# Kernel optimization log

Hardware: AMD Instinct MI355X
Metric: run time of the kernel (lower is better)

Reference implementation:

```python
import jax, jax.numpy as jnp
import numpy as np

N_NODES = 50000
N_EDGES = 800000
N_GRAPHS = 64
NEG_SLOPE = 0.2  # PyG GATConv leaky_relu default


def gat_conv(x, src, dst, W, a_src, a_dst, b, concat):
    # PyG GATConv (eval mode): h = W x -> [N,H,C]; e_ij = leakyrelu(a_src.h_j + a_dst.h_i)
    # softmax over incoming edges of each dst node; out_i = sum_j alpha_ij h_j
    N = x.shape[0]
    H, C = a_src.shape
    h = (x @ W).reshape(N, H, C)
    score_s = (h * a_src).sum(-1)  # [N,H]
    score_d = (h * a_dst).sum(-1)  # [N,H]
    e = jax.nn.leaky_relu(score_s[src] + score_d[dst], NEG_SLOPE)  # [E,H]
    m = jax.ops.segment_max(e, dst, num_segments=N)  # [N,H]
    ex = jnp.exp(e - m[dst])
    denom = jax.ops.segment_sum(ex, dst, num_segments=N)  # [N,H], >0 due to self loops
    alpha = ex / denom[dst]
    out = jax.ops.segment_sum(h[src] * alpha[..., None], dst, num_segments=N)  # [N,H,C]
    out = out.reshape(N, H * C) if concat else out.mean(axis=1)
    return out + b


def setup_inputs() -> dict:
    key = jax.random.key(0)
    ks = jax.random.split(key, 24)
    d_in, hid, heads, d_out = 16, 64, 4, 10
    hh = hid * heads

    def rn(k, shape, fan_in):
        return jax.random.normal(k, shape, dtype=jnp.float32) / np.sqrt(fan_in)

    inp = {
        "x": jax.random.normal(ks[0], (N_NODES, d_in), dtype=jnp.float32),
        "edge_index": jax.random.randint(ks[1], (2, N_EDGES), 0, N_NODES, dtype=jnp.int32),
        "batch": jnp.sort(jax.random.randint(ks[2], (N_NODES,), 0, N_GRAPHS, dtype=jnp.int32)),
        "A_W": rn(ks[3], (d_in, hid), d_in),
        "A_b": jnp.zeros((hid,), jnp.float32),
        "W0": rn(ks[4], (hid, hh), hid),
        "as0": rn(ks[5], (heads, hid), hid),
        "ad0": rn(ks[6], (heads, hid), hid),
        "b0": jnp.zeros((hh,), jnp.float32),
        "W1": rn(ks[7], (hh, hh), hh),
        "as1": rn(ks[8], (heads, hid), hid),
        "ad1": rn(ks[9], (heads, hid), hid),
        "b1": jnp.zeros((hh,), jnp.float32),
        "W2": rn(ks[10], (hh, hh), hh),
        "as2": rn(ks[11], (heads, hid), hid),
        "ad2": rn(ks[12], (heads, hid), hid),
        "b2": jnp.zeros((hid,), jnp.float32),
        "M0_W": rn(ks[13], (hid, hid), hid),
        "M0_b": jnp.zeros((hid,), jnp.float32),
        "M1_W": rn(ks[14], (hid, d_out), hid),
        "M1_b": jnp.zeros((d_out,), jnp.float32),
    }
    return inp


def reference(x, edge_index, batch, A_W, A_b, W0, as0, ad0, b0, W1, as1, ad1, b1,
              W2, as2, ad2, b2, M0_W, M0_b, M1_W, M1_b):
    N = x.shape[0]
    # sp_agg ('lrgb'): Linear(input_dim, hidden_dim)
    h = x @ A_W + A_b
    # add self loops (PyG GATConv default add_self_loops=True)
    loop = jnp.arange(N, dtype=edge_index.dtype)
    src = jnp.concatenate([edge_index[0], loop])
    dst = jnp.concatenate([edge_index[1], loop])
    # stacked GAT layers; dropout is a no-op at inference
    h = jax.nn.elu(gat_conv(h, src, dst, W0, as0, ad0, b0, concat=True))
    h = jax.nn.elu(gat_conv(h, src, dst, W1, as1, ad1, b1, concat=True))
    h = gat_conv(h, src, dst, W2, as2, ad2, b2, concat=False)
    # global mean pool over graphs
    sums = jax.ops.segment_sum(h, batch, num_segments=N_GRAPHS)
    cnts = jax.ops.segment_sum(jnp.ones((N,), h.dtype), batch, num_segments=N_GRAPHS)
    g = sums / jnp.maximum(cnts, 1.0)[:, None]
    # MLP head: Linear -> ReLU -> Linear (dropout inactive)
    g = jax.nn.relu(g @ M0_W + M0_b)
    return g @ M1_W + M1_b
```

## Files before the change

kernel.cpp:

```cpp
#include <hip/hip_runtime.h>
#include <hip/hip_bf16.h>

#define NN   50000
#define NE   800000
#define NEP  850000
#define NG   64
#define HH   256
#define DOUT 10
#define SCH  196

typedef __attribute__((ext_vector_type(8))) short bf16x8;
typedef __attribute__((ext_vector_type(4))) float f32x4;

__device__ inline float bf2f(ushort u) {
    union { unsigned int i; float f; } v; v.i = ((unsigned int)u) << 16; return v.f;
}
__device__ inline ushort f2bf(float f) {
    union { float f; unsigned int i; } v; v.f = f;
    unsigned int x = v.i;
    return (ushort)((x + 0x7FFFu + ((x >> 16) & 1u)) >> 16);
}

__global__ __launch_bounds__(256) void k_lin0b(const float* __restrict__ x,
                                               const float* __restrict__ W,
                                               const float* __restrict__ b,
                                               ushort* __restrict__ out) {
    int idx = blockIdx.x * 256 + threadIdx.x;
    int n = idx >> 6, c = idx & 63;
    if (n >= NN) return;
    float acc = b[c];
    #pragma unroll
    for (int k = 0; k < 16; ++k) acc = fmaf(x[n * 16 + k], W[k * 64 + c], acc);
    out[idx] = f2bf(acc);
}

__global__ __launch_bounds__(256) void k_degree(const int* __restrict__ ei, int* __restrict__ deg) {
    int e = blockIdx.x * 256 + threadIdx.x;
    if (e >= NEP) return;
    int dst = (e < NE) ? ei[NE + e] : (e - NE);
    atomicAdd(&deg[dst], 1);
}

__global__ __launch_bounds__(256) void k_scanA(const int* __restrict__ deg, int* __restrict__ bsum) {
    __shared__ int wsum[4];
    int b = blockIdx.x, t = threadIdx.x, lane = t & 63, w = t >> 6;
    int i = b * SCH + t;
    int v = (t < SCH && i < NN) ? deg[i] : 0;
    #pragma unroll
    for (int d = 1; d < 64; d <<= 1) v += __shfl_xor(v, d, 64);
    if (lane == 0) wsum[w] = v;
    __syncthreads();
    if (t == 0) bsum[b] = wsum[0] + wsum[1] + wsum[2] + wsum[3];
}
__global__ __launch_bounds__(256) void k_scanB(const int* __restrict__ bsum,
                                               int* __restrict__ boff,
                                               int* __restrict__ row_ptr) {
    __shared__ int wtot[4];
    int t = threadIdx.x, lane = t & 63, w = t >> 6;
    int v = bsum[t];
    int sc = v;
    #pragma unroll
    for (int d = 1; d < 64; d <<= 1) {
        int u = __shfl_up(sc, (unsigned)d, 64);
        if (lane >= d) sc += u;
    }
    if (lane == 63) wtot[w] = sc;
    __syncthreads();
    int woff = 0;
    #pragma unroll
    for (int k = 0; k < 4; ++k) woff += (k < w) ? wtot[k] : 0;
    boff[t] = woff + sc - v;
    if (t == 0) row_ptr[NN] = NEP;
}
__global__ __launch_bounds__(256) void k_scanC(const int* __restrict__ deg,
                                               const int* __restrict__ boff,
                                               int* __restrict__ row_ptr) {
    __shared__ int wtot[4];
    int b = blockIdx.x, t = threadIdx.x, lane = t & 63, w = t >> 6;
    int i = b * SCH + t;
    int v = (t < SCH && i < NN) ? deg[i] : 0;
    int sc = v;
    #pragma unroll
    for (int d = 1; d < 64; d <<= 1) {
        int u = __shfl_up(sc, (unsigned)d, 64);
        if (lane >= d) sc += u;
    }
    if (lane == 63) wtot[w] = sc;
    __syncthreads();
    int woff = 0;
    #pragma unroll
    for (int k = 0; k < 4; ++k) woff += (k < w) ? wtot[k] : 0;
    if (t < SCH && i < NN) row_ptr[i] = boff[b] + woff + sc - v;
}

__global__ __launch_bounds__(256) void k_scatter(const int* __restrict__ ei,
                                                 const int* __restrict__ row_ptr,
                                                 int* __restrict__ cursor,
                                                 int* __restrict__ col_idx) {
    int e = blockIdx.x * 256 + threadIdx.x;
    if (e >= NEP) return;
    int src, dst;
    if (e < NE) { src = ei[e]; dst = ei[NE + e]; }
    else        { src = e - NE; dst = e - NE; }
    int pos = atomicAdd(&cursor[dst], 1);
    col_idx[row_ptr[dst] + pos] = src;
}

template <int K>
__global__ __launch_bounds__(256) void k_wprep(const float* __restrict__ W,
                                               ushort* __restrict__ Whi,
                                               ushort* __restrict__ Wlo) {
    int idx = blockIdx.x * 256 + threadIdx.x;
    int k = idx >> 8, col = idx & 255;
    float v = W[idx];
    ushort hi = f2bf(v);
    Whi[col * K + k] = hi;
    Wlo[col * K + k] = f2bf(v - bf2f(hi));
}

template <int K>
__global__ __launch_bounds__(256) void k_gemm(const ushort* __restrict__ A,
                                              const ushort* __restrict__ Whi,
                                              const ushort* __restrict__ Wlo,
                                              ushort* __restrict__ C,
                                              const float* __restrict__ a_s,
                                              const float* __restrict__ a_d,
                                              float* __restrict__ ss,
                                              float* __restrict__ sd) {
    __shared__ ushort As[64][40];
    __shared__ ushort Bh[256][40];
    __shared__ ushort Bl[256][40];
    int tid = threadIdx.x;
    int w = tid >> 6, l = tid & 63;
    int rl = l & 15, rg = l >> 4;
    int m0 = blockIdx.x * 64;
    f32x4 acc[4][4];
    #pragma unroll
    for (int i = 0; i < 4; ++i)
        #pragma unroll
        for (int j = 0; j < 4; ++j) acc[i][j] = (f32x4){0.f, 0.f, 0.f, 0.f};

    int arow = tid >> 2, ak8 = (tid & 3) << 3;
    for (int k0 = 0; k0 < K; k0 += 32) {
        {
            int gr = m0 + arow; if (gr >= NN) gr = NN - 1;
            *reinterpret_cast<bf16x8*>(&As[arow][ak8]) =
                *reinterpret_cast<const bf16x8*>(&A[gr * K + k0 + ak8]);
        }
        #pragma unroll
        for (int j = 0; j < 4; ++j) {
            *reinterpret_cast<bf16x8*>(&Bh[tid][j << 3]) =
                *reinterpret_cast<const bf16x8*>(&Whi[tid * K + k0 + (j << 3)]);
            *reinterpret_cast<bf16x8*>(&Bl[tid][j << 3]) =
                *reinterpret_cast<const bf16x8*>(&Wlo[tid * K + k0 + (j << 3)]);
        }
        __syncthreads();
        int kg = rg << 3;
        bf16x8 a_frag[4], bh_frag[4], bl_frag[4];
        #pragma unroll
        for (int rt = 0; rt < 4; ++rt)
            a_frag[rt] = *reinterpret_cast<const bf16x8*>(&As[rt * 16 + rl][kg]);
        #pragma unroll
        for (int ct = 0; ct < 4; ++ct) {
            int col = (w << 6) + ct * 16 + rl;
            bh_frag[ct] = *reinterpret_cast<const bf16x8*>(&Bh[col][kg]);
            bl_frag[ct] = *reinterpret_cast<const bf16x8*>(&Bl[col][kg]);
        }
        #pragma unroll
        for (int rt = 0; rt < 4; ++rt)
            #pragma unroll
            for (int ct = 0; ct < 4; ++ct) {
                acc[rt][ct] = __builtin_amdgcn_mfma_f32_16x16x32_bf16(
                    a_frag[rt], bh_frag[ct], acc[rt][ct], 0, 0, 0);
                acc[rt][ct] = __builtin_amdgcn_mfma_f32_16x16x32_bf16(
                    a_frag[rt], bl_frag[ct], acc[rt][ct], 0, 0, 0);
            }
        __syncthreads();
    }
    float as4[4], ad4[4];
    #pragma unroll
    for (int ct = 0; ct < 4; ++ct) {
        as4[ct] = a_s[(w << 6) + ct * 16 + rl];
        ad4[ct] = a_d[(w << 6) + ct * 16 + rl];
    }
    #pragma unroll
    for (int rt = 0; rt < 4; ++rt)
        #pragma unroll
        for (int reg = 0; reg < 4; ++reg) {
            int m = m0 + rt * 16 + (rg << 2) + reg;
            float ps = 0.f, pd = 0.f;
            #pragma unroll
            for (int ct = 0; ct < 4; ++ct) {
                float v = acc[rt][ct][reg];
                ps = fmaf(v, as4[ct], ps);
                pd = fmaf(v, ad4[ct], pd);
                if (m < NN) C[m * HH + (w << 6) + ct * 16 + rl] = f2bf(v);
            }
            #pragma unroll
            for (int d = 1; d < 16; d <<= 1) {
                ps += __shfl_xor(ps, d, 64);
                pd += __shfl_xor(pd, d, 64);
            }
            if (rl == 0 && m < NN) {
                ss[m * 4 + w] = ps;
                sd[m * 4 + w] = pd;
            }
        }
}

template <int MODE>
__global__ __launch_bounds__(256) void k_agg(const ushort* __restrict__ hlin,
                                             const float* __restrict__ ss,
                                             const float* __restrict__ sd,
                                             const int* __restrict__ row_ptr,
                                             const int* __restrict__ col_idx,
                                             const float* __restrict__ bias,
                                             ushort* __restrict__ outb,
                                             float* __restrict__ outf) {
    int wid = threadIdx.x >> 6, lane = threadIdx.x & 63;
    int n = blockIdx.x * 4 + wid;
    int h = lane >> 4, c4 = (lane & 15) << 2;
    int rs = row_ptr[n], re = row_ptr[n + 1];
    float sdn = sd[n * 4 + h];
    int sn = col_idx[rs];
    float sc = ss[sn * 4 + h] + sdn;
    sc = (sc > 0.f) ? sc : 0.2f * sc;
    float m = sc, s = 1.f;
    ushort4 hv = *reinterpret_cast<const ushort4*>(&hlin[sn * HH + (h << 6) + c4]);
    float a0 = bf2f(hv.x), a1 = bf2f(hv.y), a2 = bf2f(hv.z), a3 = bf2f(hv.w);
    int e = rs + 1;
    for (; e + 1 < re; e += 2) {
        int sn0 = col_idx[e], sn1 = col_idx[e + 1];
        float t0 = ss[sn0 * 4 + h];
        float t1 = ss[sn1 * 4 + h];
        ushort4 u0 = *reinterpret_cast<const ushort4*>(&hlin[sn0 * HH + (h << 6) + c4]);
        ushort4 u1 = *reinterpret_cast<const ushort4*>(&hlin[sn1 * HH + (h << 6) + c4]);
        float s0 = t0 + sdn; s0 = (s0 > 0.f) ? s0 : 0.2f * s0;
        float mn = fmaxf(m, s0);
        float d  = __expf(fminf(m, s0) - mn);
        float cs = (s0 > m) ? d : 1.f;
        float ph = (s0 > m) ? 1.f : d;
        m = mn;
        s  = fmaf(s,  cs, ph);
        a0 = fmaf(a0, cs, ph * bf2f(u0.x));
        a1 = fmaf(a1, cs, ph * bf2f(u0.y));
        a2 = fmaf(a2, cs, ph * bf2f(u0.z));
        a3 = fmaf(a3, cs, ph * bf2f(u0.w));
        float s1 = t1 + sdn; s1 = (s1 > 0.f) ? s1 : 0.2f * s1;
        mn = fmaxf(m, s1);
        d  = __expf(fminf(m, s1) - mn);
        cs = (s1 > m) ? d : 1.f;
        ph = (s1 > m) ? 1.f : d;
        m = mn;
        s  = fmaf(s,  cs, ph);
        a0 = fmaf(a0, cs, ph * bf2f(u1.x));
        a1 = fmaf(a1, cs, ph * bf2f(u1.y));
        a2 = fmaf(a2, cs, ph * bf2f(u1.z));
        a3 = fmaf(a3, cs, ph * bf2f(u1.w));
    }
    if (e < re) {
        int sn0 = col_idx[e];
        float t0 = ss[sn0 * 4 + h];
        ushort4 u0 = *reinterpret_cast<const ushort4*>(&hlin[sn0 * HH + (h << 6) + c4]);
        float s0 = t0 + sdn; s0 = (s0 > 0.f) ? s0 : 0.2f * s0;
        float mn = fmaxf(m, s0);
        float d  = __expf(fminf(m, s0) - mn);
        float cs = (s0 > m) ? d : 1.f;
        float ph = (s0 > m) ? 1.f : d;
        s  = fmaf(s,  cs, ph);
        a0 = fmaf(a0, cs, ph * bf2f(u0.x));
        a1 = fmaf(a1, cs, ph * bf2f(u0.y));
        a2 = fmaf(a2, cs, ph * bf2f(u0.z));
        a3 = fmaf(a3, cs, ph * bf2f(u0.w));
    }
    float inv = 1.f / s;
    float o0 = a0 * inv, o1 = a1 * inv, o2 = a2 * inv, o3 = a3 * inv;
    if (MODE == 0) {
        o0 += bias[(h << 6) + c4 + 0];
        o1 += bias[(h << 6) + c4 + 1];
        o2 += bias[(h << 6) + c4 + 2];
        o3 += bias[(h << 6) + c4 + 3];
        o0 = (o0 > 0.f) ? o0 : (__expf(o0) - 1.f);
        o1 = (o1 > 0.f) ? o1 : (__expf(o1) - 1.f);
        o2 = (o2 > 0.f) ? o2 : (__expf(o2) - 1.f);
        o3 = (o3 > 0.f) ? o3 : (__expf(o3) - 1.f);
        ushort4 ob;
        ob.x = f2bf(o0); ob.y = f2bf(o1); ob.z = f2bf(o2); ob.w = f2bf(o3);
        *reinterpret_cast<ushort4*>(&outb[n * HH + (h << 6) + c4]) = ob;
    } else {
        o0 += __shfl_xor(o0, 16, 64); o0 += __shfl_xor(o0, 32, 64);
        o1 += __shfl_xor(o1, 16, 64); o1 += __shfl_xor(o1, 32, 64);
        o2 += __shfl_xor(o2, 16, 64); o2 += __shfl_xor(o2, 32, 64);
        o3 += __shfl_xor(o3, 16, 64); o3 += __shfl_xor(o3, 32, 64);
        if (h == 0) {
            float4 o = make_float4(0.25f * o0 + bias[c4 + 0],
                                   0.25f * o1 + bias[c4 + 1],
                                   0.25f * o2 + bias[c4 + 2],
                                   0.25f * o3 + bias[c4 + 3]);
            *reinterpret_cast<float4*>(&outf[n * 64 + c4]) = o;
        }
    }
}

__global__ void k_bounds(const int* __restrict__ batch, int* __restrict__ gs) {
    int g = threadIdx.x;
    if (g < NG) {
        int lo = 0, hi = NN;
        while (lo < hi) { int mid = (lo + hi) >> 1; if (batch[mid] < g) lo = mid + 1; else hi = mid; }
        gs[g] = lo;
    }
    if (g == 0) gs[NG] = NN;
}

__global__ __launch_bounds__(256) void k_poolG(const float* __restrict__ h,
                                               const int* __restrict__ gs,
                                               float* __restrict__ pool) {
    __shared__ float part[4][64];
    int g = blockIdx.x;
    int c = threadIdx.x & 63, r = threadIdx.x >> 6;
    int s = gs[g], e = gs[g + 1];
    float acc = 0.f;
    for (int n = s + r; n < e; n += 4) acc += h[n * 64 + c];
    part[r][c] = acc;
    __syncthreads();
    if (r == 0) {
        float v = part[0][c] + part[1][c] + part[2][c] + part[3][c];
        pool[g * 64 + c] = v / fmaxf((float)(e - s), 1.f);
    }
}

__global__ __launch_bounds__(256) void k_mlp(const float* __restrict__ pool,
                                             const float* __restrict__ M0W,
                                             const float* __restrict__ M0b,
                                             const float* __restrict__ M1W,
                                             const float* __restrict__ M1b,
                                             float* __restrict__ out) {
    __shared__ float g[64][64];
    __shared__ float t1[64][64];
    int tid = threadIdx.x;
    for (int idx = tid; idx < 4096; idx += 256) {
        g[idx >> 6][idx & 63] = pool[idx];
    }
    __syncthreads();
    for (int idx = tid; idx < 4096; idx += 256) {
        int i = idx >> 6, j = idx & 63;
        float acc = M0b[j];
        for (int k = 0; k < 64; ++k) acc = fmaf(g[i][k], M0W[k * 64 + j], acc);
        t1[i][j] = fmaxf(acc, 0.f);
    }
    __syncthreads();
    for (int idx = tid; idx < NG * DOUT; idx += 256) {
        int i = idx / DOUT, j = idx % DOUT;
        float acc = M1b[j];
        for (int k = 0; k < 64; ++k) acc = fmaf(t1[i][k], M1W[k * DOUT + j], acc);
        out[idx] = acc;
    }
}

extern "C" void kernel_launch(void* const* d_in, const int* in_sizes, int n_in,
                              void* d_out, int out_size, void* d_ws, size_t ws_size,
                              hipStream_t stream) {
    const float* x   = (const float*)d_in[0];
    const int*   ei  = (const int*)d_in[1];
    const int*   bat = (const int*)d_in[2];
    const float* A_W = (const float*)d_in[3];
    const float* A_b = (const float*)d_in[4];
    const float* W0  = (const float*)d_in[5];
    const float* as0 = (const float*)d_in[6];
    const float* ad0 = (const float*)d_in[7];
    const float* b0  = (const float*)d_in[8];
    const float* W1  = (const float*)d_in[9];
    const float* as1 = (const float*)d_in[10];
    const float* ad1 = (const float*)d_in[11];
    const float* b1  = (const float*)d_in[12];
    const float* W2  = (const float*)d_in[13];
    const float* as2 = (const float*)d_in[14];
    const float* ad2 = (const float*)d_in[15];
    const float* b2  = (const float*)d_in[16];
    const float* M0W = (const float*)d_in[17];
    const float* M0b = (const float*)d_in[18];
    const float* M1W = (const float*)d_in[19];
    const float* M1b = (const float*)d_in[20];

    char* ws = (char*)d_ws;
    ushort* hB_bf   = (ushort*)(ws);
    ushort* hA_bf   = (ushort*)(ws + 25600000);
    ushort* h0_bf   = (ushort*)(ws + 51200000);
    float*  h2      = (float*) (ws + 57600000);
    float*  ss      = (float*) (ws + 70400000);
    float*  sd      = (float*) (ws + 71200000);
    int*    row_ptr = (int*)   (ws + 72000000);
    int*    cursor  = (int*)   (ws + 72200064);
    int*    col_idx = (int*)   (ws + 72400128);
    float*  pool    = (float*) (ws + 75800128);
    int*    gs      = (int*)   (ws + 75816512);
    ushort* Whi     = (ushort*)(ws + 75817536);
    ushort* Wlo     = (ushort*)(ws + 75948608);
    int*    bsum    = (int*)   (ws + 76079680);
    int*    boff    = (int*)   (ws + 76080704);

    const int EB = (NEP + 255) / 256;
    const int GB = (NN + 63) / 64;

    k_lin0b<<<(NN * 64) / 256, 256, 0, stream>>>(x, A_W, A_b, h0_bf);

    hipMemsetAsync(cursor, 0, NN * sizeof(int), stream);
    k_degree<<<EB, 256, 0, stream>>>(ei, cursor);
    k_scanA<<<256, 256, 0, stream>>>(cursor, bsum);
    k_scanB<<<1, 256, 0, stream>>>(bsum, boff, row_ptr);
    k_scanC<<<256, 256, 0, stream>>>(cursor, boff, row_ptr);
    hipMemsetAsync(cursor, 0, NN * sizeof(int), stream);
    k_scatter<<<EB, 256, 0, stream>>>(ei, row_ptr, cursor, col_idx);

    k_wprep<64><<<64, 256, 0, stream>>>(W0, Whi, Wlo);
    k_gemm<64><<<GB, 256, 0, stream>>>(h0_bf, Whi, Wlo, hB_bf, as0, ad0, ss, sd);
    k_agg<0><<<12500, 256, 0, stream>>>(hB_bf, ss, sd, row_ptr, col_idx, b0, hA_bf, nullptr);
    k_wprep<256><<<256, 256, 0, stream>>>(W1, Whi, Wlo);
    k_gemm<256><<<GB, 256, 0, stream>>>(hA_bf, Whi, Wlo, hB_bf, as1, ad1, ss, sd);
    k_agg<0><<<12500, 256, 0, stream>>>(hB_bf, ss, sd, row_ptr, col_idx, b1, hA_bf, nullptr);
    k_wprep<256><<<256, 256, 0, stream>>>(W2, Whi, Wlo);
    k_gemm<256><<<GB, 256, 0, stream>>>(hA_bf, Whi, Wlo, hB_bf, as2, ad2, ss, sd);
    k_agg<1><<<12500, 256, 0, stream>>>(hB_bf, ss, sd, row_ptr, col_idx, b2, nullptr, h2);

    k_bounds<<<1, 64, 0, stream>>>(bat, gs);
    k_poolG<<<NG, 256, 0, stream>>>(h2, gs, pool);
    k_mlp<<<1, 256, 0, stream>>>(pool, M0W, M0b, M1W, M1b, (float*)d_out);
}
```

Before: 624.9 us.

## Precompute GAT softmax weights in separate kernel, simplify aggregation loop

Adds a k_alpha kernel per layer that computes each edge's attention softmax with a warp-parallel online max/sum and stores normalized fp16 weights per edge and head. The aggregation kernel then only does weighted FMAs with no per-edge exp or rescaling. The change also folds the cursor reset into k_scanC to drop one memset, and merges the graph-bounds search into k_poolG to drop one launch. In exchange it adds an extra pass over edges and score data per layer, plus an fp16 alpha buffer write and read, and lowers the precision of the attention weights.

```diff
diff --git a/kernel.cpp b/kernel.cpp
--- a/kernel.cpp
+++ b/kernel.cpp
@@ -1,5 +1,6 @@
 #include <hip/hip_runtime.h>
 #include <hip/hip_bf16.h>
+#include <hip/hip_fp16.h>
 
 #define NN   50000
 #define NE   800000
@@ -72,13 +73,14 @@
     boff[t] = woff + sc - v;
     if (t == 0) row_ptr[NN] = NEP;
 }
-__global__ __launch_bounds__(256) void k_scanC(const int* __restrict__ deg,
+__global__ __launch_bounds__(256) void k_scanC(int* __restrict__ deg,
                                                const int* __restrict__ boff,
                                                int* __restrict__ row_ptr) {
     __shared__ int wtot[4];
     int b = blockIdx.x, t = threadIdx.x, lane = t & 63, w = t >> 6;
     int i = b * SCH + t;
-    int v = (t < SCH && i < NN) ? deg[i] : 0;
+    bool live = (t < SCH && i < NN);
+    int v = live ? deg[i] : 0;
     int sc = v;
     #pragma unroll
     for (int d = 1; d < 64; d <<= 1) {
@@ -90,7 +92,7 @@
     int woff = 0;
     #pragma unroll
     for (int k = 0; k < 4; ++k) woff += (k < w) ? wtot[k] : 0;
-    if (t < SCH && i < NN) row_ptr[i] = boff[b] + woff + sc - v;
+    if (live) { row_ptr[i] = boff[b] + woff + sc - v; deg[i] = 0; }
 }
 
 __global__ __launch_bounds__(256) void k_scatter(const int* __restrict__ ei,
@@ -208,10 +210,70 @@
         }
 }
 
+__global__ __launch_bounds__(256) void k_alpha(const float* __restrict__ ss,
+                                               const float* __restrict__ sd,
+                                               const int* __restrict__ row_ptr,
+                                               const int* __restrict__ col_idx,
+                                               ushort* __restrict__ alp) {
+    int wid = threadIdx.x >> 6, lane = threadIdx.x & 63;
+    int n = blockIdx.x * 4 + wid;
+    int rs = row_ptr[n], re = row_ptr[n + 1];
+    float4 sdn = *reinterpret_cast<const float4*>(&sd[n * 4]);
+    float m0 = -1e30f, m1 = -1e30f, m2 = -1e30f, m3 = -1e30f;
+    float s0 = 0.f, s1 = 0.f, s2 = 0.f, s3 = 0.f;
+    for (int e = rs + lane; e < re; e += 64) {
+        int sn = col_idx[e];
+        float4 t = *reinterpret_cast<const float4*>(&ss[sn * 4]);
+        float c0 = t.x + sdn.x; c0 = (c0 > 0.f) ? c0 : 0.2f * c0;
+        float c1 = t.y + sdn.y; c1 = (c1 > 0.f) ? c1 : 0.2f * c1;
+        float c2 = t.z + sdn.z; c2 = (c2 > 0.f) ? c2 : 0.2f * c2;
+        float c3 = t.w + sdn.w; c3 = (c3 > 0.f) ? c3 : 0.2f * c3;
+        float mn, d;
+        mn = fmaxf(m0, c0); d = __expf(fminf(m0, c0) - mn);
+        s0 = (c0 > m0) ? fmaf(s0, d, 1.f) : (s0 + d); m0 = mn;
+        mn = fmaxf(m1, c1); d = __expf(fminf(m1, c1) - mn);
+        s1 = (c1 > m1) ? fmaf(s1, d, 1.f) : (s1 + d); m1 = mn;
+        mn = fmaxf(m2, c2); d = __expf(fminf(m2, c2) - mn);
+        s2 = (c2 > m2) ? fmaf(s2, d, 1.f) : (s2 + d); m2 = mn;
+        mn = fmaxf(m3, c3); d = __expf(fminf(m3, c3) - mn);
+        s3 = (c3 > m3) ? fmaf(s3, d, 1.f) : (s3 + d); m3 = mn;
+    }
+    #pragma unroll
+    for (int dd = 1; dd < 64; dd <<= 1) {
+        float mo, so, mn, f;
+        mo = __shfl_xor(m0, dd, 64); so = __shfl_xor(s0, dd, 64);
+        mn = fmaxf(m0, mo); f = __expf(fminf(m0, mo) - mn);
+        s0 = (m0 >= mo) ? fmaf(so, f, s0) : fmaf(s0, f, so); m0 = mn;
+        mo = __shfl_xor(m1, dd, 64); so = __shfl_xor(s1, dd, 64);
+        mn = fmaxf(m1, mo); f = __expf(fminf(m1, mo) - mn);
+        s1 = (m1 >= mo) ? fmaf(so, f, s1) : fmaf(s1, f, so); m1 = mn;
+        mo = __shfl_xor(m2, dd, 64); so = __shfl_xor(s2, dd, 64);
+        mn = fmaxf(m2, mo); f = __expf(fminf(m2, mo) - mn);
+        s2 = (m2 >= mo) ? fmaf(so, f, s2) : fmaf(s2, f, so); m2 = mn;
+        mo = __shfl_xor(m3, dd, 64); so = __shfl_xor(s3, dd, 64);
+        mn = fmaxf(m3, mo); f = __expf(fminf(m3, mo) - mn);
+        s3 = (m3 >= mo) ? fmaf(so, f, s3) : fmaf(s3, f, so); m3 = mn;
+    }
+    float is0 = 1.f / s0, is1 = 1.f / s1, is2 = 1.f / s2, is3 = 1.f / s3;
+    for (int e = rs + lane; e < re; e += 64) {
+        int sn = col_idx[e];
+        float4 t = *reinterpret_cast<const float4*>(&ss[sn * 4]);
+        float c0 = t.x + sdn.x; c0 = (c0 > 0.f) ? c0 : 0.2f * c0;
+        float c1 = t.y + sdn.y; c1 = (c1 > 0.f) ? c1 : 0.2f * c1;
+        float c2 = t.z + sdn.z; c2 = (c2 > 0.f) ? c2 : 0.2f * c2;
+        float c3 = t.w + sdn.w; c3 = (c3 > 0.f) ? c3 : 0.2f * c3;
+        ushort4 o;
+        o.x = __half_as_ushort(__float2half(__expf(c0 - m0) * is0));
+        o.y = __half_as_ushort(__float2half(__expf(c1 - m1) * is1));
+        o.z = __half_as_ushort(__float2half(__expf(c2 - m2) * is2));
+        o.w = __half_as_ushort(__float2half(__expf(c3 - m3) * is3));
+        *reinterpret_cast<ushort4*>(&alp[e * 4]) = o;
+    }
+}
+
 template <int MODE>
 __global__ __launch_bounds__(256) void k_agg(const ushort* __restrict__ hlin,
-                                             const float* __restrict__ ss,
-                                             const float* __restrict__ sd,
+                                             const ushort* __restrict__ alp,
                                              const int* __restrict__ row_ptr,
                                              const int* __restrict__ col_idx,
                                              const float* __restrict__ bias,
@@ -221,65 +283,37 @@
     int n = blockIdx.x * 4 + wid;
     int h = lane >> 4, c4 = (lane & 15) << 2;
     int rs = row_ptr[n], re = row_ptr[n + 1];
-    float sdn = sd[n * 4 + h];
-    int sn = col_idx[rs];
-    float sc = ss[sn * 4 + h] + sdn;
-    sc = (sc > 0.f) ? sc : 0.2f * sc;
-    float m = sc, s = 1.f;
-    ushort4 hv = *reinterpret_cast<const ushort4*>(&hlin[sn * HH + (h << 6) + c4]);
-    float a0 = bf2f(hv.x), a1 = bf2f(hv.y), a2 = bf2f(hv.z), a3 = bf2f(hv.w);
-    int e = rs + 1;
+    float a0 = 0.f, a1 = 0.f, a2 = 0.f, a3 = 0.f;
+    int e = rs;
     for (; e + 1 < re; e += 2) {
         int sn0 = col_idx[e], sn1 = col_idx[e + 1];
-        float t0 = ss[sn0 * 4 + h];
-        float t1 = ss[sn1 * 4 + h];
+        float al0 = __half2float(__ushort_as_half(alp[e * 4 + h]));
+        float al1 = __half2float(__ushort_as_half(alp[(e + 1) * 4 + h]));
         ushort4 u0 = *reinterpret_cast<const ushort4*>(&hlin[sn0 * HH + (h << 6) + c4]);
         ushort4 u1 = *reinterpret_cast<const ushort4*>(&hlin[sn1 * HH + (h << 6) + c4]);
-        float s0 = t0 + sdn; s0 = (s0 > 0.f) ? s0 : 0.2f * s0;
-        float mn = fmaxf(m, s0);
-        float d  = __expf(fminf(m, s0) - mn);
-        float cs = (s0 > m) ? d : 1.f;
-        float ph = (s0 > m) ? 1.f : d;
-        m = mn;
-        s  = fmaf(s,  cs, ph);
-        a0 = fmaf(a0, cs, ph * bf2f(u0.x));
-        a1 = fmaf(a1, cs, ph * bf2f(u0.y));
-        a2 = fmaf(a2, cs, ph * bf2f(u0.z));
-        a3 = fmaf(a3, cs, ph * bf2f(u0.w));
-        float s1 = t1 + sdn; s1 = (s1 > 0.f) ? s1 : 0.2f * s1;
-        mn = fmaxf(m, s1);
-        d  = __expf(fminf(m, s1) - mn);
-        cs = (s1 > m) ? d : 1.f;
-        ph = (s1 > m) ? 1.f : d;
-        m = mn;
-        s  = fmaf(s,  cs, ph);
-        a0 = fmaf(a0, cs, ph * bf2f(u1.x));
-        a1 = fmaf(a1, cs, ph * bf2f(u1.y));
-        a2 = fmaf(a2, cs, ph * bf2f(u1.z));
-        a3 = fmaf(a3, cs, ph * bf2f(u1.w));
+        a0 = fmaf(al0, bf2f(u0.x), a0);
+        a1 = fmaf(al0, bf2f(u0.y), a1);
+        a2 = fmaf(al0, bf2f(u0.z), a2);
+        a3 = fmaf(al0, bf2f(u0.w), a3);
+        a0 = fmaf(al1, bf2f(u1.x), a0);
+        a1 = fmaf(al1, bf2f(u1.y), a1);
+        a2 = fmaf(al1, bf2f(u1.z), a2);
+        a3 = fmaf(al1, bf2f(u1.w), a3);
     }
     if (e < re) {
         int sn0 = col_idx[e];
-        float t0 = ss[sn0 * 4 + h];
+        float al0 = __half2float(__ushort_as_half(alp[e * 4 + h]));
         ushort4 u0 = *reinterpret_cast<const ushort4*>(&hlin[sn0 * HH + (h << 6) + c4]);
-        float s0 = t0 + sdn; s0 = (s0 > 0.f) ? s0 : 0.2f * s0;
-        float mn = fmaxf(m, s0);
-        float d  = __expf(fminf(m, s0) - mn);
-        float cs = (s0 > m) ? d : 1.f;
-        float ph = (s0 > m) ? 1.f : d;
-        s  = fmaf(s,  cs, ph);
-        a0 = fmaf(a0, cs, ph * bf2f(u0.x));
-        a1 = fmaf(a1, cs, ph * bf2f(u0.y));
-        a2 = fmaf(a2, cs, ph * bf2f(u0.z));
-        a3 = fmaf(a3, cs, ph * bf2f(u0.w));
-    }
-    float inv = 1.f / s;
-    float o0 = a0 * inv, o1 = a1 * inv, o2 = a2 * inv, o3 = a3 * inv;
+        a0 = fmaf(al0, bf2f(u0.x), a0);
+        a1 = fmaf(al0, bf2f(u0.y), a1);
+        a2 = fmaf(al0, bf2f(u0.z), a2);
+        a3 = fmaf(al0, bf2f(u0.w), a3);
+    }
     if (MODE == 0) {
-        o0 += bias[(h << 6) + c4 + 0];
-        o1 += bias[(h << 6) + c4 + 1];
-        o2 += bias[(h << 6) + c4 + 2];
-        o3 += bias[(h << 6) + c4 + 3];
+        float o0 = a0 + bias[(h << 6) + c4 + 0];
+        float o1 = a1 + bias[(h << 6) + c4 + 1];
+        float o2 = a2 + bias[(h << 6) + c4 + 2];
+        float o3 = a3 + bias[(h << 6) + c4 + 3];
         o0 = (o0 > 0.f) ? o0 : (__expf(o0) - 1.f);
         o1 = (o1 > 0.f) ? o1 : (__expf(o1) - 1.f);
         o2 = (o2 > 0.f) ? o2 : (__expf(o2) - 1.f);
@@ -288,37 +322,32 @@
         ob.x = f2bf(o0); ob.y = f2bf(o1); ob.z = f2bf(o2); ob.w = f2bf(o3);
         *reinterpret_cast<ushort4*>(&outb[n * HH + (h << 6) + c4]) = ob;
     } else {
-        o0 += __shfl_xor(o0, 16, 64); o0 += __shfl_xor(o0, 32, 64);
-        o1 += __shfl_xor(o1, 16, 64); o1 += __shfl_xor(o1, 32, 64);
-        o2 += __shfl_xor(o2, 16, 64); o2 += __shfl_xor(o2, 32, 64);
-        o3 += __shfl_xor(o3, 16, 64); o3 += __shfl_xor(o3, 32, 64);
+        a0 += __shfl_xor(a0, 16, 64); a0 += __shfl_xor(a0, 32, 64);
+        a1 += __shfl_xor(a1, 16, 64); a1 += __shfl_xor(a1, 32, 64);
+        a2 += __shfl_xor(a2, 16, 64); a2 += __shfl_xor(a2, 32, 64);
+        a3 += __shfl_xor(a3, 16, 64); a3 += __shfl_xor(a3, 32, 64);
         if (h == 0) {
-            float4 o = make_float4(0.25f * o0 + bias[c4 + 0],
-                                   0.25f * o1 + bias[c4 + 1],
-                                   0.25f * o2 + bias[c4 + 2],
-                                   0.25f * o3 + bias[c4 + 3]);
+            float4 o = make_float4(0.25f * a0 + bias[c4 + 0],
+                                   0.25f * a1 + bias[c4 + 1],
+                                   0.25f * a2 + bias[c4 + 2],
+                                   0.25f * a3 + bias[c4 + 3]);
             *reinterpret_cast<float4*>(&outf[n * 64 + c4]) = o;
         }
     }
 }
 
-__global__ void k_bounds(const int* __restrict__ batch, int* __restrict__ gs) {
-    int g = threadIdx.x;
-    if (g < NG) {
-        int lo = 0, hi = NN;
-        while (lo < hi) { int mid = (lo + hi) >> 1; if (batch[mid] < g) lo = mid + 1; else hi = mid; }
-        gs[g] = lo;
-    }
-    if (g == 0) gs[NG] = NN;
-}
-
 __global__ __launch_bounds__(256) void k_poolG(const float* __restrict__ h,
-                                               const int* __restrict__ gs,
+                                               const int* __restrict__ batch,
                                                float* __restrict__ pool) {
     __shared__ float part[4][64];
     int g = blockIdx.x;
+    int lo = 0, hi = NN;
+    while (lo < hi) { int mid = (lo + hi) >> 1; if (batch[mid] < g) lo = mid + 1; else hi = mid; }
+    int s = lo;
+    lo = 0; hi = NN;
+    while (lo < hi) { int mid = (lo + hi) >> 1; if (batch[mid] < g + 1) lo = mid + 1; else hi = mid; }
+    int e = lo;
     int c = threadIdx.x & 63, r = threadIdx.x >> 6;
-    int s = gs[g], e = gs[g + 1];
     float acc = 0.f;
     for (int n = s + r; n < e; n += 4) acc += h[n * 64 + c];
     part[r][c] = acc;
@@ -393,11 +422,11 @@
     int*    cursor  = (int*)   (ws + 72200064);
     int*    col_idx = (int*)   (ws + 72400128);
     float*  pool    = (float*) (ws + 75800128);
-    int*    gs      = (int*)   (ws + 75816512);
     ushort* Whi     = (ushort*)(ws + 75817536);
     ushort* Wlo     = (ushort*)(ws + 75948608);
     int*    bsum    = (int*)   (ws + 76079680);
     int*    boff    = (int*)   (ws + 76080704);
+    ushort* alp     = (ushort*)(ws + 76081728);
 
     const int EB = (NEP + 255) / 256;
     const int GB = (NN + 63) / 64;
@@ -409,20 +438,21 @@
     k_scanA<<<256, 256, 0, stream>>>(cursor, bsum);
     k_scanB<<<1, 256, 0, stream>>>(bsum, boff, row_ptr);
     k_scanC<<<256, 256, 0, stream>>>(cursor, boff, row_ptr);
-    hipMemsetAsync(cursor, 0, NN * sizeof(int), stream);
     k_scatter<<<EB, 256, 0, stream>>>(ei, row_ptr, cursor, col_idx);
 
     k_wprep<64><<<64, 256, 0, stream>>>(W0, Whi, Wlo);
     k_gemm<64><<<GB, 256, 0, stream>>>(h0_bf, Whi, Wlo, hB_bf, as0, ad0, ss, sd);
-    k_agg<0><<<12500, 256, 0, stream>>>(hB_bf, ss, sd, row_ptr, col_idx, b0, hA_bf, nullptr);
+    k_alpha<<<12500, 256, 0, stream>>>(ss, sd, row_ptr, col_idx, alp);
+    k_agg<0><<<12500, 256, 0, stream>>>(hB_bf, alp, row_ptr, col_idx, b0, hA_bf, nullptr);
     k_wprep<256><<<256, 256, 0, stream>>>(W1, Whi, Wlo);
     k_gemm<256><<<GB, 256, 0, stream>>>(hA_bf, Whi, Wlo, hB_bf, as1, ad1, ss, sd);
-    k_agg<0><<<12500, 256, 0, stream>>>(hB_bf, ss, sd, row_ptr, col_idx, b1, hA_bf, nullptr);
+    k_alpha<<<12500, 256, 0, stream>>>(ss, sd, row_ptr, col_idx, alp);
+    k_agg<0><<<12500, 256, 0, stream>>>(hB_bf, alp, row_ptr, col_idx, b1, hA_bf, nullptr);
     k_wprep<256><<<256, 256, 0, stream>>>(W2, Whi, Wlo);
     k_gemm<256><<<GB, 256, 0, stream>>>(hA_bf, Whi, Wlo, hB_bf, as2, ad2, ss, sd);
-    k_agg<1><<<12500, 256, 0, stream>>>(hB_bf, ss, sd, row_ptr, col_idx, b2, nullptr, h2);
-
-    k_bounds<<<1, 64, 0, stream>>>(bat, gs);
-    k_poolG<<<NG, 256, 0, stream>>>(h2, gs, pool);
+    k_alpha<<<12500, 256, 0, stream>>>(ss, sd, row_ptr, col_idx, alp);
+    k_agg<1><<<12500, 256, 0, stream>>>(hB_bf, alp, row_ptr, col_idx, b2, nullptr, h2);
+
+    k_poolG<<<NG, 256, 0, stream>>>(h2, bat, pool);
     k_mlp<<<1, 256, 0, stream>>>(pool, M0W, M0b, M1W, M1b, (float*)d_out);
 }
```

Result: slower. 693.7 us (+11.0%).
